# Performance work log

Hardware: AMD Instinct MI355X
Metric: run time of the kernel (lower is better)

The kernel has to match this reference:

```python
import jax, jax.numpy as jnp
import numpy as np

N_NODES = 50000
N_EDGES = 600000
D_IN = 128
D_OUT = 128
K_HOPS = 2  # Gra_inc(2)


def _gcn_norm(edge_index, edge_weight, num_nodes, dtype):
    # Add self-loops (weight 1.0) and compute symmetric GCN normalization.
    loop = jnp.arange(num_nodes, dtype=edge_index.dtype)
    row = jnp.concatenate([edge_index[0], loop])  # source
    col = jnp.concatenate([edge_index[1], loop])  # destination
    w = jnp.concatenate([edge_weight, jnp.ones((num_nodes,), dtype=dtype)])
    deg = jax.ops.segment_sum(w, col, num_segments=num_nodes)
    dinv = jnp.where(deg > 0, jax.lax.rsqrt(deg), jnp.zeros_like(deg))
    norm = dinv[row] * w * dinv[col]  # [E + N]
    return row, col, norm


def setup_inputs() -> dict:
    key = jax.random.key(0)
    k1, k2, k3, k4 = jax.random.split(key, 4)
    x = jax.random.normal(k1, (N_NODES, D_IN), dtype=jnp.float32)
    edge_index = jax.random.randint(k2, (2, N_EDGES), 0, N_NODES, dtype=jnp.int64)
    edge_weight = jax.random.uniform(k3, (N_EDGES,), dtype=jnp.float32)
    # Linear(in,out,bias=False) weight, PyTorch layout [out, in]
    W = jax.random.normal(k4, (D_OUT, D_IN), dtype=jnp.float32) * (1.0 / np.sqrt(D_IN))
    return {"x": x, "edge_index": edge_index, "edge_weight": edge_weight, "W": W}


def reference(x, edge_index, edge_weight, W):
    num_nodes = x.shape[0]
    h = x @ W.T  # lin11: [N, D_OUT]
    row, col, norm = _gcn_norm(edge_index, edge_weight, num_nodes, h.dtype)
    # Gra_inc(2): K=2 hops of normalized sparse propagation h <- A_hat @ h
    for _ in range(K_HOPS):
        msgs = norm[:, None] * h[row]  # gather + scale, [E+N, D_OUT]
        h = jax.ops.segment_sum(msgs, col, num_segments=num_nodes)
    return h  # bias is None (bias=False)
```

## Files before the change

### kernel.cpp

```cpp
#include <hip/hip_runtime.h>

typedef unsigned long long u64;
typedef unsigned int u32;
typedef _Float16 f16;

#define NN 50000
#define NE 600000
#define D  128
#define NWAVE 3125
#define GB 196
#define GSTRIDE 784
#define EPB 2048
#define NB_P 293
#define NP 196
#define MAXCAP 3584
#define NSTRIP 2
#define GS 1563

typedef __attribute__((ext_vector_type(8))) __bf16 bf16x8;
typedef __attribute__((ext_vector_type(8))) unsigned short us8;
typedef __attribute__((ext_vector_type(8))) f16 f16x8;
typedef __attribute__((ext_vector_type(4))) float f32x4;

__device__ __forceinline__ unsigned short f2bf(float f) {
    u32 u = __float_as_uint(f);
    return (unsigned short)((u + 0x7FFFu + ((u >> 16) & 1u)) >> 16);
}
__device__ __forceinline__ float bf2f(unsigned short h) {
    return __uint_as_float((u32)h << 16);
}

__global__ __launch_bounds__(256) void wprep(const float* __restrict__ W,
                                             us8* __restrict__ Whi,
                                             us8* __restrict__ Wlo,
                                             int* __restrict__ pcur) {
    const int i = blockIdx.x * 256 + threadIdx.x;
    if (i < NP) pcur[i] = i * MAXCAP;
    if (i < 2048) {
        const int ln = i & 63, nt = (i >> 6) & 7, kc4 = i >> 9;
        const float* p =
            W + (size_t)(nt * 16 + (ln & 15)) * D + kc4 * 32 + (ln >> 4) * 8;
        float v[8];
        *(float4*)&v[0] = *(const float4*)p;
        *(float4*)&v[4] = *(const float4*)(p + 4);
        us8 hi, lo;
#pragma unroll
        for (int j = 0; j < 8; ++j) {
            const unsigned short hb = f2bf(v[j]);
            hi[j] = hb;
            lo[j] = f2bf(v[j] - bf2f(hb));
        }
        Whi[i] = hi;
        Wlo[i] = lo;
    }
}

__global__ __launch_bounds__(256) void gemm_scatter(
    const float* __restrict__ x, const us8* __restrict__ Whi,
    const us8* __restrict__ Wlo, f16* __restrict__ h16,
    const int* __restrict__ row, const int* __restrict__ col,
    const float* __restrict__ w, int* __restrict__ pcur,
    u64* __restrict__ part) {
    const int t = threadIdx.x;
    __shared__ us8 WH[2048];
    __shared__ us8 WL[2048];

    if (blockIdx.x < NB_P) {
        int* bins = (int*)WH;
        int* off0 = bins + 256;
        int* cur  = off0 + 256;
        for (int i = t; i < NP; i += 256) { bins[i] = 0; cur[i] = 0; }
        __syncthreads();
        const int e0 = blockIdx.x * EPB + t;
        int cc[8];
#pragma unroll
        for (int s = 0; s < 8; ++s) {
            const int e = e0 + s * 256;
            cc[s] = (e < NE) ? col[e] : -1;
            if (cc[s] >= 0) atomicAdd(&bins[cc[s] >> 8], 1);
        }
        __syncthreads();
        for (int i = t; i < NP; i += 256)
            off0[i] = bins[i] ? atomicAdd(&pcur[i], bins[i]) : 0;
        __syncthreads();
#pragma unroll
        for (int s = 0; s < 8; ++s) {
            const int e = e0 + s * 256;
            if (e < NE) {
                const int c = cc[s];
                const int p = c >> 8;
                const int lr = atomicAdd(&cur[p], 1);
                part[off0[p] + lr] = ((u64)__float_as_uint(w[e]) << 32) |
                                     ((u32)row[e] << 8) | (u32)(c & 255);
            }
        }
        return;
    }

    const int wid = (blockIdx.x - NB_P) * 4 + (t >> 6);
    const int lane = t & 63;
    const int l15 = lane & 15, l4 = lane >> 4;

    int g = (wid < NWAVE) ? wid : NWAVE - 1;
    const float* px = x + (size_t)(g * 16 + l15) * D + l4 * 8;
    float4 ar[8];
#pragma unroll
    for (int c = 0; c < 4; ++c) {
        ar[2 * c]     = *(const float4*)(px + c * 32);
        ar[2 * c + 1] = *(const float4*)(px + c * 32 + 4);
    }

#pragma unroll
    for (int i = 0; i < 8; ++i) {
        WH[t + i * 256] = Whi[t + i * 256];
        WL[t + i * 256] = Wlo[t + i * 256];
    }
    __syncthreads();

#pragma unroll
    for (int l = 0; l < 4; ++l) {
        float4 an[8];
        int gn = wid + (l + 1) * GSTRIDE;
        if (gn >= NWAVE) gn = NWAVE - 1;
        if (l < 3) {
            const float* pn = x + (size_t)(gn * 16 + l15) * D + l4 * 8;
#pragma unroll
            for (int c = 0; c < 4; ++c) {
                an[2 * c]     = *(const float4*)(pn + c * 32);
                an[2 * c + 1] = *(const float4*)(pn + c * 32 + 4);
            }
        }

        f32x4 acc[8];
#pragma unroll
        for (int nt = 0; nt < 8; ++nt) acc[nt] = (f32x4){0.f, 0.f, 0.f, 0.f};

#pragma unroll
        for (int c = 0; c < 4; ++c) {
            float v[8];
            *(float4*)&v[0] = ar[2 * c];
            *(float4*)&v[4] = ar[2 * c + 1];
            us8 hiu, lou;
#pragma unroll
            for (int j = 0; j < 8; ++j) {
                const unsigned short hb = f2bf(v[j]);
                hiu[j] = hb;
                lou[j] = f2bf(v[j] - bf2f(hb));
            }
            const bf16x8 ah = *(const bf16x8*)&hiu;
            const bf16x8 al = *(const bf16x8*)&lou;
#pragma unroll
            for (int nt = 0; nt < 8; ++nt) {
                const bf16x8 bh = *(const bf16x8*)&WH[c * 512 + nt * 64 + lane];
                const bf16x8 bl = *(const bf16x8*)&WL[c * 512 + nt * 64 + lane];
                acc[nt] = __builtin_amdgcn_mfma_f32_16x16x32_bf16(ah, bh, acc[nt], 0, 0, 0);
                acc[nt] = __builtin_amdgcn_mfma_f32_16x16x32_bf16(al, bh, acc[nt], 0, 0, 0);
                acc[nt] = __builtin_amdgcn_mfma_f32_16x16x32_bf16(ah, bl, acc[nt], 0, 0, 0);
            }
        }

        const int row0 = g * 16;
#pragma unroll
        for (int nt = 0; nt < 8; ++nt) {
            f16* o = h16 + (size_t)(nt >> 2) * ((size_t)NN * 64) +
                     (nt & 3) * 16 + l15;
#pragma unroll
            for (int r = 0; r < 4; ++r)
                o[(size_t)(row0 + l4 * 4 + r) * 64] = (f16)acc[nt][r];
        }

        g = gn;
#pragma unroll
        for (int i = 0; i < 8; ++i) ar[i] = an[i];
    }
}

__global__ __launch_bounds__(256) void csr_k(
    const u64* __restrict__ part, const int* __restrict__ pcur,
    int* __restrict__ base, int* __restrict__ kcnt,
    float* __restrict__ dinv, int2* __restrict__ sedge) {
    __shared__ u32 cntQ[4][256];
    __shared__ int curQ[4][256];
    __shared__ float wsL[256];
    __shared__ int sw[256];
    const int p = blockIdx.x, tid = threadIdx.x;
    const int eb = p * MAXCAP, ee = pcur[p];

#pragma unroll
    for (int q = 0; q < 4; ++q) cntQ[q][tid] = 0u;
    wsL[tid] = 0.f;
    __syncthreads();
    for (int e = eb + tid; e < ee; e += 256) {
        const u64 pk = part[e];
        const int cl = (int)(pk & 255u);
        const int r = (int)((pk >> 8) & 0xFFFFu);
        const int q = (r >= 37500) ? 3 : (r >= 25000) ? 2 : (r >= 12500) ? 1 : 0;
        atomicAdd(&cntQ[q][cl], 1u);
        atomicAdd(&wsL[cl], __uint_as_float((u32)(pk >> 32)));
    }
    __syncthreads();

    const int node = p * 256 + tid;
    const float di = rsqrtf(1.0f + wsL[tid]);
    const int c0 = (int)cntQ[0][tid], c1 = (int)cntQ[1][tid];
    const int c2 = (int)cntQ[2][tid], c3 = (int)cntQ[3][tid];
    const int myc = c0 + c1 + c2 + c3;
    sw[tid] = myc;
    __syncthreads();
    for (int off = 1; off < 256; off <<= 1) {
        int tv = (tid >= off) ? sw[tid - off] : 0;
        __syncthreads();
        if (tid >= off) sw[tid] += tv;
        __syncthreads();
    }
    const int excl = sw[tid] - myc;
    if (node < NN) {
        dinv[node] = di;
        base[node] = eb + excl;
        kcnt[node] = myc;
    }
    __syncthreads();
    wsL[tid] = di;
    curQ[0][tid] = excl;
    curQ[1][tid] = excl + c0;
    curQ[2][tid] = excl + c0 + c1;
    curQ[3][tid] = excl + c0 + c1 + c2;
    __syncthreads();

    for (int e = eb + tid; e < ee; e += 256) {
        const u64 pk = part[e];
        const int cl = (int)(pk & 255u);
        const int r = (int)((pk >> 8) & 0xFFFFu);
        const int q = (r >= 37500) ? 3 : (r >= 25000) ? 2 : (r >= 12500) ? 1 : 0;
        const float wv = __uint_as_float((u32)(pk >> 32));
        const int lr = atomicAdd(&curQ[q][cl], 1);
        int2 ed;
        ed.x = r;
        ed.y = __float_as_int(wv * wsL[cl]);
        sedge[eb + lr] = ed;
    }
}

template <int OUTF>
__global__ __launch_bounds__(256) void hop_kernel(
    const f16* __restrict__ src, f16* __restrict__ dst16,
    float* __restrict__ dstf, const int2* __restrict__ sedge,
    const int* __restrict__ base, const int* __restrict__ kcnt,
    const float* __restrict__ dinv) {
    const int node = blockIdx.x * 32 + (threadIdx.x >> 3);
    if (node >= NN) return;
    const int strip = blockIdx.y;
    const int lo8 = (threadIdx.x & 7) * 8;
    const f16* hs = src + (size_t)strip * ((size_t)NN * 64) + lo8;

    const int b = base[node];
    const int k = kcnt[node];

    float acc[8] = {0.f, 0.f, 0.f, 0.f, 0.f, 0.f, 0.f, 0.f};
#pragma unroll 4
    for (int j = 0; j < k; ++j) {
        const int2 ed = sedge[b + j];
        const f16x8 hv = *(const f16x8*)(hs + (size_t)ed.x * 64);
        const float nm = __int_as_float(ed.y) * dinv[ed.x];
#pragma unroll
        for (int i = 0; i < 8; ++i) acc[i] = fmaf(nm, (float)hv[i], acc[i]);
    }
    const float di = dinv[node];
    const float d2 = di * di;
    const f16x8 sv = *(const f16x8*)(hs + (size_t)node * 64);
#pragma unroll
    for (int i = 0; i < 8; ++i) acc[i] = fmaf(d2, (float)sv[i], acc[i]);

    if (OUTF) {
        float* o = dstf + (size_t)node * D + strip * 64 + lo8;
        *(float4*)&o[0] = make_float4(acc[0], acc[1], acc[2], acc[3]);
        *(float4*)&o[4] = make_float4(acc[4], acc[5], acc[6], acc[7]);
    } else {
        f16x8 ov;
#pragma unroll
        for (int i = 0; i < 8; ++i) ov[i] = (f16)acc[i];
        *(f16x8*)(dst16 + (size_t)strip * ((size_t)NN * 64) + (size_t)node * 64 + lo8) = ov;
    }
}

extern "C" void kernel_launch(void* const* d_in, const int* in_sizes, int n_in,
                              void* d_out, int out_size, void* d_ws,
                              size_t ws_size, hipStream_t stream) {
    const float* x  = (const float*)d_in[0];
    const int*   ei = (const int*)d_in[1];
    const float* w  = (const float*)d_in[2];
    const float* W  = (const float*)d_in[3];
    float* out = (float*)d_out;

    const int* row = ei;
    const int* col = ei + NE;

    f16* h16a = (f16*)d_ws;
    f16* h16b = h16a + (size_t)2 * NN * 64;
    u64* part = (u64*)h16b;
    us8* Whi = (us8*)(h16b + (size_t)2 * NN * 64);
    us8* Wlo = Whi + 2048;
    int* pcur = (int*)(Wlo + 2048);
    int* base = pcur + NP;
    int* kcnt = base + NN;
    float* dinv = (float*)(kcnt + NN);
    int2* sedge = (int2*)(dinv + NN);

    wprep<<<8, 256, 0, stream>>>(W, Whi, Wlo, pcur);
    gemm_scatter<<<NB_P + GB, 256, 0, stream>>>(x, Whi, Wlo, h16a, row, col,
                                                w, pcur, part);
    csr_k<<<NP, 256, 0, stream>>>(part, pcur, base, kcnt, dinv, sedge);

    hop_kernel<0><<<dim3(GS, NSTRIP), 256, 0, stream>>>(h16a, h16b, nullptr,
                                                        sedge, base, kcnt, dinv);
    hop_kernel<1><<<dim3(GS, NSTRIP), 256, 0, stream>>>(h16b, nullptr, out,
                                                        sedge, base, kcnt, dinv);
}
```

Measured before the change: 90.74 us.

## Fold W split into GEMM, stage partitions in LDS, hoist dinv scaling

Removes the separate wprep kernel. Each GEMM block now converts W into bf16 hi/lo parts directly into shared memory, and the partition cursors are zeroed with a memset, with offsets made absolute at the write site. The CSR build copies each partition's packed edges into LDS once instead of reading global memory twice. The per-edge destination dinv multiply moves out of the edge weights into a single per-node scale in the hop kernel. The aim is fewer launches and less global traffic and arithmetic. The cost is that every GEMM block repeats the W conversion, and csr_k uses more LDS per block.

```diff
diff --git a/kernel.cpp b/kernel.cpp
--- a/kernel.cpp
+++ b/kernel.cpp
@@ -30,37 +30,11 @@
     return __uint_as_float((u32)h << 16);
 }
 
-__global__ __launch_bounds__(256) void wprep(const float* __restrict__ W,
-                                             us8* __restrict__ Whi,
-                                             us8* __restrict__ Wlo,
-                                             int* __restrict__ pcur) {
-    const int i = blockIdx.x * 256 + threadIdx.x;
-    if (i < NP) pcur[i] = i * MAXCAP;
-    if (i < 2048) {
-        const int ln = i & 63, nt = (i >> 6) & 7, kc4 = i >> 9;
-        const float* p =
-            W + (size_t)(nt * 16 + (ln & 15)) * D + kc4 * 32 + (ln >> 4) * 8;
-        float v[8];
-        *(float4*)&v[0] = *(const float4*)p;
-        *(float4*)&v[4] = *(const float4*)(p + 4);
-        us8 hi, lo;
-#pragma unroll
-        for (int j = 0; j < 8; ++j) {
-            const unsigned short hb = f2bf(v[j]);
-            hi[j] = hb;
-            lo[j] = f2bf(v[j] - bf2f(hb));
-        }
-        Whi[i] = hi;
-        Wlo[i] = lo;
-    }
-}
-
 __global__ __launch_bounds__(256) void gemm_scatter(
-    const float* __restrict__ x, const us8* __restrict__ Whi,
-    const us8* __restrict__ Wlo, f16* __restrict__ h16,
-    const int* __restrict__ row, const int* __restrict__ col,
-    const float* __restrict__ w, int* __restrict__ pcur,
-    u64* __restrict__ part) {
+    const float* __restrict__ x, const float* __restrict__ W,
+    f16* __restrict__ h16, const int* __restrict__ row,
+    const int* __restrict__ col, const float* __restrict__ w,
+    int* __restrict__ pcur, u64* __restrict__ part) {
     const int t = threadIdx.x;
     __shared__ us8 WH[2048];
     __shared__ us8 WL[2048];
@@ -90,8 +64,9 @@
                 const int c = cc[s];
                 const int p = c >> 8;
                 const int lr = atomicAdd(&cur[p], 1);
-                part[off0[p] + lr] = ((u64)__float_as_uint(w[e]) << 32) |
-                                     ((u32)row[e] << 8) | (u32)(c & 255);
+                part[(size_t)p * MAXCAP + off0[p] + lr] =
+                    ((u64)__float_as_uint(w[e]) << 32) |
+                    ((u32)row[e] << 8) | (u32)(c & 255);
             }
         }
         return;
@@ -111,9 +86,23 @@
     }
 
 #pragma unroll
-    for (int i = 0; i < 8; ++i) {
-        WH[t + i * 256] = Whi[t + i * 256];
-        WL[t + i * 256] = Wlo[t + i * 256];
+    for (int s = 0; s < 8; ++s) {
+        const int i = s * 256 + t;
+        const int ln = i & 63, ntt = (i >> 6) & 7, kc4 = i >> 9;
+        const float* pw =
+            W + (size_t)(ntt * 16 + (ln & 15)) * D + kc4 * 32 + (ln >> 4) * 8;
+        float v[8];
+        *(float4*)&v[0] = *(const float4*)pw;
+        *(float4*)&v[4] = *(const float4*)(pw + 4);
+        us8 hi, lo;
+#pragma unroll
+        for (int j = 0; j < 8; ++j) {
+            const unsigned short hb = f2bf(v[j]);
+            hi[j] = hb;
+            lo[j] = f2bf(v[j] - bf2f(hb));
+        }
+        WH[i] = hi;
+        WL[i] = lo;
     }
     __syncthreads();
 
@@ -179,19 +168,22 @@
     const u64* __restrict__ part, const int* __restrict__ pcur,
     int* __restrict__ base, int* __restrict__ kcnt,
     float* __restrict__ dinv, int2* __restrict__ sedge) {
+    __shared__ u64 eL[MAXCAP];
     __shared__ u32 cntQ[4][256];
     __shared__ int curQ[4][256];
     __shared__ float wsL[256];
     __shared__ int sw[256];
     const int p = blockIdx.x, tid = threadIdx.x;
-    const int eb = p * MAXCAP, ee = pcur[p];
-
+    const int ne = pcur[p];
+    const u64* ps = part + (size_t)p * MAXCAP;
+
+    for (int j = tid; j < ne; j += 256) eL[j] = ps[j];
 #pragma unroll
     for (int q = 0; q < 4; ++q) cntQ[q][tid] = 0u;
     wsL[tid] = 0.f;
     __syncthreads();
-    for (int e = eb + tid; e < ee; e += 256) {
-        const u64 pk = part[e];
+    for (int j = tid; j < ne; j += 256) {
+        const u64 pk = eL[j];
         const int cl = (int)(pk & 255u);
         const int r = (int)((pk >> 8) & 0xFFFFu);
         const int q = (r >= 37500) ? 3 : (r >= 25000) ? 2 : (r >= 12500) ? 1 : 0;
@@ -216,28 +208,25 @@
     const int excl = sw[tid] - myc;
     if (node < NN) {
         dinv[node] = di;
-        base[node] = eb + excl;
+        base[node] = p * MAXCAP + excl;
         kcnt[node] = myc;
     }
-    __syncthreads();
-    wsL[tid] = di;
     curQ[0][tid] = excl;
     curQ[1][tid] = excl + c0;
     curQ[2][tid] = excl + c0 + c1;
     curQ[3][tid] = excl + c0 + c1 + c2;
     __syncthreads();
 
-    for (int e = eb + tid; e < ee; e += 256) {
-        const u64 pk = part[e];
+    for (int j = tid; j < ne; j += 256) {
+        const u64 pk = eL[j];
         const int cl = (int)(pk & 255u);
         const int r = (int)((pk >> 8) & 0xFFFFu);
         const int q = (r >= 37500) ? 3 : (r >= 25000) ? 2 : (r >= 12500) ? 1 : 0;
-        const float wv = __uint_as_float((u32)(pk >> 32));
         const int lr = atomicAdd(&curQ[q][cl], 1);
         int2 ed;
         ed.x = r;
-        ed.y = __float_as_int(wv * wsL[cl]);
-        sedge[eb + lr] = ed;
+        ed.y = (int)(u32)(pk >> 32);
+        sedge[(size_t)p * MAXCAP + lr] = ed;
     }
 }
 
@@ -269,7 +258,7 @@
     const float d2 = di * di;
     const f16x8 sv = *(const f16x8*)(hs + (size_t)node * 64);
 #pragma unroll
-    for (int i = 0; i < 8; ++i) acc[i] = fmaf(d2, (float)sv[i], acc[i]);
+    for (int i = 0; i < 8; ++i) acc[i] = fmaf(d2, (float)sv[i], di * acc[i]);
 
     if (OUTF) {
         float* o = dstf + (size_t)node * D + strip * 64 + lo8;
@@ -298,17 +287,15 @@
     f16* h16a = (f16*)d_ws;
     f16* h16b = h16a + (size_t)2 * NN * 64;
     u64* part = (u64*)h16b;
-    us8* Whi = (us8*)(h16b + (size_t)2 * NN * 64);
-    us8* Wlo = Whi + 2048;
-    int* pcur = (int*)(Wlo + 2048);
+    int* pcur = (int*)(h16b + (size_t)2 * NN * 64);
     int* base = pcur + NP;
     int* kcnt = base + NN;
     float* dinv = (float*)(kcnt + NN);
     int2* sedge = (int2*)(dinv + NN);
 
-    wprep<<<8, 256, 0, stream>>>(W, Whi, Wlo, pcur);
-    gemm_scatter<<<NB_P + GB, 256, 0, stream>>>(x, Whi, Wlo, h16a, row, col,
-                                                w, pcur, part);
+    hipMemsetAsync(pcur, 0, (size_t)NP * sizeof(int), stream);
+    gemm_scatter<<<NB_P + GB, 256, 0, stream>>>(x, W, h16a, row, col, w,
+                                                pcur, part);
     csr_k<<<NP, 256, 0, stream>>>(part, pcur, base, kcnt, dinv, sedge);
 
     hop_kernel<0><<<dim3(GS, NSTRIP), 256, 0, stream>>>(h16a, h16b, nullptr,
```

New measurement: 92.92 us. +2.4%, slower.
